# Kernel tuning notes

Hardware: AMD Instinct MI355X
Metric: run time of the kernel (lower is better)

The kernel has to match this reference:

```python
import jax, jax.numpy as jnp
import numpy as np

B, IN, H, OUT, RANK = 2048, 256, 128, 128, 8
EPS = 1e-5

def setup_inputs() -> dict:
    key = jax.random.key(0)
    ks = jax.random.split(key, 9)
    inv = lambda n: 1.0 / np.sqrt(n)
    return {
        "X": jax.random.normal(ks[0], (B, IN), jnp.float32),
        "W1": jax.random.uniform(ks[1], (IN, H), jnp.float32, -inv(IN), inv(IN)),
        "b1": jnp.zeros((H,), jnp.float32),
        "W2": jax.random.uniform(ks[2], (IN, OUT), jnp.float32, -inv(IN), inv(IN)),
        "b2": jnp.zeros((OUT,), jnp.float32),
        "W3": jax.random.uniform(ks[3], (H, OUT), jnp.float32, -inv(H), inv(H)),
        "b3": jnp.zeros((OUT,), jnp.float32),
        "P": jax.random.normal(ks[4], (RANK, H, H, H), jnp.float32),  # (rank, p, q, k)
        "gz": jnp.ones((H,), jnp.float32),
        "bz": jnp.zeros((H,), jnp.float32),
        "gy": jnp.ones((H,), jnp.float32),
        "by": jnp.zeros((H,), jnp.float32),
    }

def _bn(x, g, b):
    # training-mode BatchNorm1d: batch stats, biased variance
    m = x.mean(axis=0)
    v = x.var(axis=0)
    return (x - m) * jax.lax.rsqrt(v + EPS) * g + b

def reference(X, W1, b1, W2, b2, W3, b3, P, gz, bz, gy, by):
    Z = jax.nn.relu(X @ W1 + b1)               # (B, H); dropout = identity (eval)

    def step(carry, Pi):
        Zi, Y = carry
        # batch_quadratic: out[b,k] = sum_{p,q} Zi[b,p] * Pi[p,q,k] * Z[b,q]
        Zi = jnp.einsum('bp,pqk,bq->bk', Zi, Pi, Z)
        Zi = _bn(Zi, gz, bz)
        return (Zi, Y + Zi / RANK), None

    Y0 = jnp.zeros((X.shape[0], H), X.dtype)
    (_, Y), _ = jax.lax.scan(step, (Z, Y0), P)
    Y = _bn(Y, gy, by)
    out = jax.nn.relu(jax.nn.relu(Y @ W3 + b3) + jax.nn.relu(X @ W2 + b2))
    return out
```

## Files before the change

kernel.cpp:

```cpp
#include <hip/hip_runtime.h>

typedef __bf16 bf16x8 __attribute__((ext_vector_type(8)));
typedef float  floatx4 __attribute__((ext_vector_type(4)));

constexpr int B_    = 2048;
constexpr int NIN   = 256;
constexpr int H_    = 128;
constexpr int RANK_ = 8;
constexpr float EPS_ = 1e-5f;

__global__ __launch_bounds__(256)
void k_head(const float* __restrict__ X,
            const float* __restrict__ W1, const float* __restrict__ b1,
            const float* __restrict__ W2, const float* __restrict__ b2,
            const float* __restrict__ P,
            float* __restrict__ R2, __bf16* __restrict__ Zbf,
            __bf16* __restrict__ Pperm, float* __restrict__ stats ) {
    __shared__ float smem[4160];
    const int bx = blockIdx.x, t = threadIdx.x;

    if (bx < RANK_ + 1) stats[bx * 256 + t] = 0.f;

    {
        const int b0 = bx * 2;
#pragma unroll
        for (int i = 0; i < 2; ++i) {
            const int e = i * 256 + t;
            smem[e] = X[(size_t)(b0 + (e >> 8)) * NIN + (e & 255)];
        }
        __syncthreads();
        const int col = t & 127, rh = t >> 7;
        float s1 = 0.f, s2 = 0.f;
        const float* sx = smem + rh * 256;
#pragma unroll 16
        for (int i = 0; i < NIN; ++i) {
            const float w1 = W1[i * H_ + col];
            const float w2 = W2[i * H_ + col];
            s1 = fmaf(sx[i], w1, s1);  s2 = fmaf(sx[i], w2, s2);
        }
        const int br = b0 + rh;
        const float z = fmaxf(s1 + b1[col], 0.f), r = fmaxf(s2 + b2[col], 0.f);
        Zbf[(size_t)br * H_ + col] = (__bf16)z;  R2[(size_t)br * H_ + col] = r;
        __syncthreads();
    }
    {
        const int r = bx >> 7, p = bx & 127;
        const float4* Pp4 = (const float4*)(P + ((size_t)r * H_ + p) * (H_ * H_));
        __bf16* dst = Pperm + (size_t)r * (H_ * H_ * H_);
        const int L = t & 63, quad = L >> 4, lo = L & 15, g0 = t >> 6;

        float4 rg[4][4];
#pragma unroll
        for (int s = 0; s < 4; ++s)
#pragma unroll
            for (int it = 0; it < 4; ++it) {
                const int idx = it * 256 + t;
                rg[s][it] = Pp4[(size_t)(s * 32 + (idx >> 5)) * 32 + (idx & 31)];
            }
#pragma unroll
        for (int s = 0; s < 4; ++s) {
            if (s) __syncthreads();
#pragma unroll
            for (int it = 0; it < 4; ++it) {
                const int idx = it * 256 + t;
                float* d = smem + (idx >> 5) * 129 + (idx & 31) * 4;
                d[0] = rg[s][it].x; d[1] = rg[s][it].y;
                d[2] = rg[s][it].z; d[3] = rg[s][it].w;
            }
            __syncthreads();
#pragma unroll
            for (int gg = 0; gg < 2; ++gg) {
                const int g = g0 + 4 * gg;
                __bf16 v8[8];
#pragma unroll
                for (int j = 0; j < 8; ++j)
                    v8[j] = (__bf16)smem[(quad * 8 + j) * 129 + g * 16 + lo];
                *(bf16x8*)(dst + (((size_t)(g * 128 + p) * 4 + s) * 64 + L) * 8) =
                    *(const bf16x8*)v8;
            }
        }
    }
}

__global__ __launch_bounds__(512, 2)
void k_rank(const __bf16* __restrict__ Pr, const __bf16* __restrict__ Zbf,
            const float* __restrict__ prevT, const float* __restrict__ prevPart,
            const float* __restrict__ gz, const float* __restrict__ bz,
            float* __restrict__ T, float* __restrict__ ownPart, const int first) {
    __shared__ float smem[8960];
    const int kg = blockIdx.x, mblk = blockIdx.y, b0 = mblk * 64;
    const int t = threadIdx.x;
    const int w = t >> 6, L = t & 63, quad = L >> 4, lo = L & 15;

    float* sAl = smem + 8704; float* sBe = smem + 8832;
    bf16x8 A[4][4];
#pragma unroll
    for (int mt = 0; mt < 4; ++mt)
#pragma unroll
        for (int ks = 0; ks < 4; ++ks)
            A[mt][ks] = *(const bf16x8*)(Zbf + (size_t)(b0 + mt * 16 + lo) * H_ + ks * 32 + quad * 8);

    const bf16x8* Pb = (const bf16x8*)Pr;
    const int p0 = w * 16;
    const size_t fbase = ((size_t)kg * 128 + p0) * 4;

#define LOADB(dst, pl) do {                                                   \
    _Pragma("unroll") for (int s_ = 0; s_ < 4; ++s_)                          \
        dst[s_] = Pb[(fbase + (size_t)(pl) * 4 + s_) * 64 + L];               \
} while (0)

    bf16x8 B0[4], B1[4], B2[4], B3[4];
    LOADB(B0, 0);
    LOADB(B1, 1);
    LOADB(B2, 2);
    LOADB(B3, 3);

    if (!first && t < 128) {
        float s1 = 0.f, s2 = 0.f;
#pragma unroll 8
        for (int m = 0; m < 32; ++m) {
            s1 += prevPart[m * 128 + t];
            s2 += prevPart[(32 + m) * 128 + t];
        }
        const float mm = s1 * (1.f / B_);
        const float var = s2 * (1.f / B_) - mm * mm;
        const float a = rsqrtf(var + EPS_) * gz[t];
        sAl[t] = a; sBe[t] = bz[t] - mm * a;
    }
    __syncthreads();
    {
        const int cg = t >> 4, rs = t & 15;
        if (first) {
#pragma unroll
            for (int i = 0; i < 4; ++i) {
                const int row = rs + 16 * i;
                const ushort4 u = *(const ushort4*)(Zbf + (size_t)(b0 + row) * H_ + cg * 4);
                smem[(cg * 4 + 0) * 68 + row] = __uint_as_float((unsigned)u.x << 16);
                smem[(cg * 4 + 1) * 68 + row] = __uint_as_float((unsigned)u.y << 16);
                smem[(cg * 4 + 2) * 68 + row] = __uint_as_float((unsigned)u.z << 16);
                smem[(cg * 4 + 3) * 68 + row] = __uint_as_float((unsigned)u.w << 16);
            }
        } else {
            const float4 al4 = *(const float4*)&sAl[cg * 4];
            const float4 be4 = *(const float4*)&sBe[cg * 4];
#pragma unroll
            for (int i = 0; i < 4; ++i) {
                const int row = rs + 16 * i;
                const float4 v = *(const float4*)(prevT + (size_t)(b0 + row) * H_ + cg * 4);
                smem[(cg * 4 + 0) * 68 + row] = fmaf(v.x, al4.x, be4.x);
                smem[(cg * 4 + 1) * 68 + row] = fmaf(v.y, al4.y, be4.y);
                smem[(cg * 4 + 2) * 68 + row] = fmaf(v.z, al4.z, be4.z);
                smem[(cg * 4 + 3) * 68 + row] = fmaf(v.w, al4.w, be4.w);
            }
        }
    }
    __syncthreads();

    floatx4 acc[4];
#pragma unroll
    for (int mt = 0; mt < 4; ++mt) acc[mt] = (floatx4){0.f, 0.f, 0.f, 0.f};

#define COMPUTE(Bx, pg) do {                                                  \
    floatx4 S_[4];                                                            \
    __builtin_amdgcn_s_setprio(1);                                            \
    _Pragma("unroll") for (int mt_ = 0; mt_ < 4; ++mt_)                       \
        S_[mt_] = __builtin_amdgcn_mfma_f32_16x16x32_bf16(                    \
            A[mt_][0], Bx[0], (floatx4){0.f, 0.f, 0.f, 0.f}, 0, 0, 0);        \
    _Pragma("unroll") for (int ks_ = 1; ks_ < 4; ++ks_)                       \
        _Pragma("unroll") for (int mt_ = 0; mt_ < 4; ++mt_)                   \
            S_[mt_] = __builtin_amdgcn_mfma_f32_16x16x32_bf16(                \
                A[mt_][ks_], Bx[ks_], S_[mt_], 0, 0, 0);                      \
    __builtin_amdgcn_s_setprio(0);                                            \
    _Pragma("unroll") for (int mt_ = 0; mt_ < 4; ++mt_) {                     \
        const floatx4 zi_ =                                                   \
            *(const floatx4*)&smem[(pg) * 68 + mt_ * 16 + quad * 4];          \
        acc[mt_] += zi_ * S_[mt_];                                            \
    }                                                                         \
} while (0)

#pragma unroll
    for (int pp = 0; pp < 16; pp += 4) {
        COMPUTE(B0, p0 + pp);     if (pp < 12) LOADB(B0, pp + 4);
        COMPUTE(B1, p0 + pp + 1); if (pp < 12) LOADB(B1, pp + 5);
        COMPUTE(B2, p0 + pp + 2); if (pp < 12) LOADB(B2, pp + 6);
        COMPUTE(B3, p0 + pp + 3); if (pp < 12) LOADB(B3, pp + 7);
    }
#undef LOADB
#undef COMPUTE

    __syncthreads();
#pragma unroll
    for (int mt = 0; mt < 4; ++mt)
#pragma unroll
        for (int i = 0; i < 4; ++i)
            smem[w * 1024 + (mt * 4 + i) * 64 + L] = acc[mt][i];
    if (t < 32) smem[8192 + t] = 0.f;
    __syncthreads();

    float cs = 0.f, cs2 = 0.f;
#pragma unroll
    for (int k2 = 0; k2 < 2; ++k2) {
        const int e = t + 512 * k2;
        float v = 0.f;
#pragma unroll
        for (int q = 0; q < 8; ++q) v += smem[q * 1024 + e];
        const int j = e >> 6, L2 = e & 63;
        const int row = b0 + (j >> 2) * 16 + (L2 >> 4) * 4 + (j & 3);
        const int col = kg * 16 + (L2 & 15);
        T[(size_t)row * H_ + col] = v;
        cs += v; cs2 += v * v;
    }
    cs  += __shfl_xor(cs, 16);  cs  += __shfl_xor(cs, 32);
    cs2 += __shfl_xor(cs2, 16); cs2 += __shfl_xor(cs2, 32);
    if (L < 16) { atomicAdd(&smem[8192 + L], cs); atomicAdd(&smem[8208 + L], cs2); }
    __syncthreads();
    if (t < 16)      ownPart[(size_t)mblk * 128 + kg * 16 + t]        = smem[8192 + t];
    else if (t < 32) ownPart[(size_t)(32 + mblk) * 128 + kg * 16 + t - 16] = smem[8192 + t];
}

__global__ __launch_bounds__(256)
void k_y(const float* __restrict__ T, const float* __restrict__ partials,
         const float* __restrict__ gz, const float* __restrict__ bz,
         float* __restrict__ Y, float* __restrict__ ysums) {
    __shared__ float al[1024], be[1024], red[256];
    const int bx = blockIdx.x, t = threadIdx.x;
    for (int e = t; e < 1024; e += 256) {
        const int rr = e >> 7, k = e & 127;
        const float* bp = partials + (size_t)rr * 8192;
        float s1 = 0.f, s2 = 0.f;
#pragma unroll 8
        for (int m = 0; m < 32; ++m) {
            s1 += bp[m * 128 + k];
            s2 += bp[(32 + m) * 128 + k];
        }
        const float mm = s1 * (1.f / B_);
        const float var = s2 * (1.f / B_) - mm * mm;
        const float a = rsqrtf(var + EPS_) * gz[k];
        al[e] = a; be[e] = bz[k] - mm * a;
    }
    red[t] = 0.f;
    __syncthreads();
    const int col = t & 127, half = t >> 7;
    float ps = 0.f, ps2 = 0.f;
    for (int i = 0; i < 16; ++i) {
        const int b = bx * 32 + half + 2 * i;
        float y = 0.f;
#pragma unroll
        for (int rr = 0; rr < 8; ++rr)
            y += fmaf(T[(size_t)rr * B_ * H_ + (size_t)b * H_ + col],
                      al[rr * 128 + col], be[rr * 128 + col]);
        y *= (1.f / RANK_);
        Y[(size_t)b * H_ + col] = y;
        ps += y; ps2 += y * y;
    }
    atomicAdd(&red[col],       half == 0 ? ps  : 0.f);
    atomicAdd(&red[128 + col], half == 0 ? ps2 : 0.f);
    __syncthreads();
    atomicAdd(&red[col],       half == 1 ? ps  : 0.f);
    atomicAdd(&red[128 + col], half == 1 ? ps2 : 0.f);
    __syncthreads();
    if (t < 128) {
        atomicAdd(&ysums[t],       red[t]);
        atomicAdd(&ysums[128 + t], red[128 + t]);
    }
}

__global__ __launch_bounds__(256)
void k_out(const float* __restrict__ Y, const float* __restrict__ ystats,
           const float* __restrict__ gy, const float* __restrict__ by,
           const float* __restrict__ W3, const float* __restrict__ b3,
           const float* __restrict__ R2, float* __restrict__ out) {
    __shared__ float sy[8 * 132];
    const int bx = blockIdx.x, t = threadIdx.x;
    const int col = t & 127, rh = t >> 7;
    const int b0 = bx * 8;
    const float mm = ystats[col] * (1.f / B_);
    const float var = ystats[128 + col] * (1.f / B_) - mm * mm;
    const float ay = rsqrtf(var + EPS_) * gy[col];
    const float bb = by[col] - mm * ay;
#pragma unroll
    for (int i = 0; i < 4; ++i) {
        const int row = rh + 2 * i;
        sy[row * 132 + col] = fmaf(Y[(size_t)(b0 + row) * H_ + col], ay, bb);
    }
    __syncthreads();
#pragma unroll
    for (int j = 0; j < 4; ++j) {
        const int row = rh * 4 + j;
        float s = 0.f;
        const float* syr = sy + row * 132;
#pragma unroll 8
        for (int h = 0; h < H_; ++h)
            s = fmaf(syr[h], W3[h * H_ + col], s);
        const size_t gi = (size_t)(b0 + row) * H_ + col;
        out[gi] = fmaxf(fmaxf(s + b3[col], 0.f) + R2[gi], 0.f);
    }
}

extern "C" void kernel_launch(void* const* d_in, const int* in_sizes, int n_in,
                              void* d_out, int out_size, void* d_ws, size_t ws_size,
                              hipStream_t stream) {
    const float* X  = (const float*)d_in[0];
    const float* W1 = (const float*)d_in[1];
    const float* b1 = (const float*)d_in[2];
    const float* W2 = (const float*)d_in[3];
    const float* b2 = (const float*)d_in[4];
    const float* W3 = (const float*)d_in[5];
    const float* b3 = (const float*)d_in[6];
    const float* P  = (const float*)d_in[7];
    const float* gz = (const float*)d_in[8];
    const float* bz = (const float*)d_in[9];
    const float* gy = (const float*)d_in[10];
    const float* by = (const float*)d_in[11];
    float* out = (float*)d_out;

    const size_t rankElems = (size_t)H_ * H_ * H_;

    char* wsb = (char*)d_ws;
    float* R2       = (float*)wsb;   wsb += (size_t)B_ * H_ * 4;
    float* Y        = (float*)wsb;   wsb += (size_t)B_ * H_ * 4;
    float* stats    = (float*)wsb;   wsb += (size_t)(RANK_ + 1) * 256 * 4;
    float* partials = (float*)wsb;   wsb += (size_t)RANK_ * 2 * 32 * 128 * 4;
    float* T        = (float*)wsb;   wsb += (size_t)RANK_ * B_ * H_ * 4;
    __bf16* Zbf     = (__bf16*)wsb;  wsb += (size_t)B_ * H_ * 2;
    __bf16* Pperm   = (__bf16*)wsb;

    float* ysums = stats + RANK_ * 256;

    k_head<<<1024, 256, 0, stream>>>(X, W1, b1, W2, b2, P, R2, Zbf, Pperm, stats);

    for (int r = 0; r < RANK_; ++r) {
        const float* prevT = (r == 0) ? (const float*)Zbf : (T + (size_t)(r - 1) * B_ * H_);
        const float* prevP = (r == 0) ? partials : (partials + (size_t)(r - 1) * 8192);
        k_rank<<<dim3(8, 32), 512, 0, stream>>>(Pperm + (size_t)r * rankElems, Zbf,
                                                prevT, prevP, gz, bz,
                                                T + (size_t)r * B_ * H_,
                                                partials + (size_t)r * 8192,
                                                r == 0 ? 1 : 0);
    }

    k_y<<<64, 256, 0, stream>>>(T, partials, gz, bz, Y, ysums);
    k_out<<<256, 256, 0, stream>>>(Y, ysums, gy, by, W3, b3, R2, out);
}
```

Before: 285.5 us.

## Split P permutation across 4x more blocks and simplify k_rank input staging

k_head now launches 4096 blocks, each converting one quarter (one s-slice) of a P row to bf16 instead of looping over all four slices in one block. The X@W1/W2 head work stays on the first 1024 blocks. This raises parallelism and cuts register pressure on the dominant P conversion pass. Separately, k_rank's staging of Z/prevT into shared memory switches from vectorized 4-wide loads to scalar per-column loads with a different thread mapping. That may improve LDS store conflicts but reduces global load width.

```diff
diff --git a/kernel.cpp b/kernel.cpp
--- a/kernel.cpp
+++ b/kernel.cpp
@@ -21,7 +21,7 @@
 
     if (bx < RANK_ + 1) stats[bx * 256 + t] = 0.f;
 
-    {
+    if (bx < 1024) {
         const int b0 = bx * 2;
 #pragma unroll
         for (int i = 0; i < 2; ++i) {
@@ -44,40 +44,34 @@
         __syncthreads();
     }
     {
-        const int r = bx >> 7, p = bx & 127;
+        const int r = bx >> 9, p = (bx >> 2) & 127, s = bx & 3;
         const float4* Pp4 = (const float4*)(P + ((size_t)r * H_ + p) * (H_ * H_));
         __bf16* dst = Pperm + (size_t)r * (H_ * H_ * H_);
         const int L = t & 63, quad = L >> 4, lo = L & 15, g0 = t >> 6;
 
-        float4 rg[4][4];
-#pragma unroll
-        for (int s = 0; s < 4; ++s)
-#pragma unroll
-            for (int it = 0; it < 4; ++it) {
-                const int idx = it * 256 + t;
-                rg[s][it] = Pp4[(size_t)(s * 32 + (idx >> 5)) * 32 + (idx & 31)];
-            }
-#pragma unroll
-        for (int s = 0; s < 4; ++s) {
-            if (s) __syncthreads();
-#pragma unroll
-            for (int it = 0; it < 4; ++it) {
-                const int idx = it * 256 + t;
-                float* d = smem + (idx >> 5) * 129 + (idx & 31) * 4;
-                d[0] = rg[s][it].x; d[1] = rg[s][it].y;
-                d[2] = rg[s][it].z; d[3] = rg[s][it].w;
-            }
-            __syncthreads();
-#pragma unroll
-            for (int gg = 0; gg < 2; ++gg) {
-                const int g = g0 + 4 * gg;
-                __bf16 v8[8];
-#pragma unroll
-                for (int j = 0; j < 8; ++j)
-                    v8[j] = (__bf16)smem[(quad * 8 + j) * 129 + g * 16 + lo];
-                *(bf16x8*)(dst + (((size_t)(g * 128 + p) * 4 + s) * 64 + L) * 8) =
-                    *(const bf16x8*)v8;
-            }
+        float4 rg[4];
+#pragma unroll
+        for (int it = 0; it < 4; ++it) {
+            const int idx = it * 256 + t;
+            rg[it] = Pp4[(size_t)(s * 32 + (idx >> 5)) * 32 + (idx & 31)];
+        }
+#pragma unroll
+        for (int it = 0; it < 4; ++it) {
+            const int idx = it * 256 + t;
+            float* d = smem + (idx >> 5) * 129 + (idx & 31) * 4;
+            d[0] = rg[it].x; d[1] = rg[it].y;
+            d[2] = rg[it].z; d[3] = rg[it].w;
+        }
+        __syncthreads();
+#pragma unroll
+        for (int gg = 0; gg < 2; ++gg) {
+            const int g = g0 + 4 * gg;
+            __bf16 v8[8];
+#pragma unroll
+            for (int j = 0; j < 8; ++j)
+                v8[j] = (__bf16)smem[(quad * 8 + j) * 129 + g * 16 + lo];
+            *(bf16x8*)(dst + (((size_t)(g * 128 + p) * 4 + s) * 64 + L) * 8) =
+                *(const bf16x8*)v8;
         }
     }
 }
@@ -129,28 +123,19 @@
     }
     __syncthreads();
     {
-        const int cg = t >> 4, rs = t & 15;
+        const int sp = t & 127, rr = t >> 7;
         if (first) {
 #pragma unroll
-            for (int i = 0; i < 4; ++i) {
-                const int row = rs + 16 * i;
-                const ushort4 u = *(const ushort4*)(Zbf + (size_t)(b0 + row) * H_ + cg * 4);
-                smem[(cg * 4 + 0) * 68 + row] = __uint_as_float((unsigned)u.x << 16);
-                smem[(cg * 4 + 1) * 68 + row] = __uint_as_float((unsigned)u.y << 16);
-                smem[(cg * 4 + 2) * 68 + row] = __uint_as_float((unsigned)u.z << 16);
-                smem[(cg * 4 + 3) * 68 + row] = __uint_as_float((unsigned)u.w << 16);
+            for (int i = 0; i < 16; ++i) {
+                const int row = rr + 4 * i;
+                smem[sp * 68 + row] = (float)Zbf[(size_t)(b0 + row) * H_ + sp];
             }
         } else {
-            const float4 al4 = *(const float4*)&sAl[cg * 4];
-            const float4 be4 = *(const float4*)&sBe[cg * 4];
-#pragma unroll
-            for (int i = 0; i < 4; ++i) {
-                const int row = rs + 16 * i;
-                const float4 v = *(const float4*)(prevT + (size_t)(b0 + row) * H_ + cg * 4);
-                smem[(cg * 4 + 0) * 68 + row] = fmaf(v.x, al4.x, be4.x);
-                smem[(cg * 4 + 1) * 68 + row] = fmaf(v.y, al4.y, be4.y);
-                smem[(cg * 4 + 2) * 68 + row] = fmaf(v.z, al4.z, be4.z);
-                smem[(cg * 4 + 3) * 68 + row] = fmaf(v.w, al4.w, be4.w);
+            const float a = sAl[sp], be = sBe[sp];
+#pragma unroll
+            for (int i = 0; i < 16; ++i) {
+                const int row = rr + 4 * i;
+                smem[sp * 68 + row] = fmaf(prevT[(size_t)(b0 + row) * H_ + sp], a, be);
             }
         }
     }
@@ -214,7 +199,7 @@
     cs2 += __shfl_xor(cs2, 16); cs2 += __shfl_xor(cs2, 32);
     if (L < 16) { atomicAdd(&smem[8192 + L], cs); atomicAdd(&smem[8208 + L], cs2); }
     __syncthreads();
-    if (t < 16)      ownPart[(size_t)mblk * 128 + kg * 16 + t]        = smem[8192 + t];
+    if (t < 16)      ownPart[(size_t)mblk * 128 + kg * 16 + t]             = smem[8192 + t];
     else if (t < 32) ownPart[(size_t)(32 + mblk) * 128 + kg * 16 + t - 16] = smem[8192 + t];
 }
 
@@ -327,7 +312,7 @@
 
     float* ysums = stats + RANK_ * 256;
 
-    k_head<<<1024, 256, 0, stream>>>(X, W1, b1, W2, b2, P, R2, Zbf, Pperm, stats);
+    k_head<<<4096, 256, 0, stream>>>(X, W1, b1, W2, b2, P, R2, Zbf, Pperm, stats);
 
     for (int r = 0; r < RANK_; ++r) {
         const float* prevT = (r == 0) ? (const float*)Zbf : (T + (size_t)(r - 1) * B_ * H_);
```

New measurement: 282.5 us. About the same (-1.1%).
